# Optimization experiments

Measured on AMD Instinct MI355X. Metric: run time of the kernel, lower is better.

Reference implementation:

```python
import jax, jax.numpy as jnp
import numpy as np

N, F, E, LIN, C, B = 16384, 500, 128, 128, 10, 4096
P_EDGE = 0.002  # ~32 avg degree


def _l2norm(x):
    # F.normalize(dim=1), eps=1e-12
    n = jnp.linalg.norm(x, axis=1, keepdims=True)
    return x / jnp.maximum(n, 1e-12)


def setup_inputs() -> dict:
    key = jax.random.key(0)
    ks = jax.random.split(key, 10)
    adj = (jax.random.uniform(ks[0], (N, N)) < P_EDGE).astype(jnp.float32)
    idx = jnp.arange(N)
    adj = adj.at[idx, idx].set(1.0)  # self-loops guarantee degree >= 1
    data = jax.random.normal(ks[1], (N, F), dtype=jnp.float32)
    nodes = jax.random.randint(ks[2], (B,), 0, N)
    # Encoder 1: Linear(2F -> E); Encoder 2: Linear(2E -> E); classifier heads
    W1 = jax.random.normal(ks[3], (E, 2 * F), dtype=jnp.float32) * 0.03
    b1 = jnp.zeros((E,), jnp.float32)
    W2 = jax.random.normal(ks[4], (E, 2 * E), dtype=jnp.float32) * 0.06
    b2 = jnp.zeros((E,), jnp.float32)
    Wl1 = jax.random.normal(ks[5], (LIN, E), dtype=jnp.float32) * 0.08
    bl1 = jnp.zeros((LIN,), jnp.float32)
    Wl2 = jax.random.normal(ks[6], (C, LIN), dtype=jnp.float32) * 0.12
    bl2 = jnp.zeros((C,), jnp.float32)
    return {"nodes": nodes, "adj": adj, "data": data,
            "W1": W1, "b1": b1, "W2": W2, "b2": b2,
            "Wl1": Wl1, "bl1": bl1, "Wl2": Wl2, "bl2": bl2}


def reference(nodes, adj, data, W1, b1, W2, b2, Wl1, bl1, Wl2, bl2):
    deg = jnp.sum(adj, axis=1, keepdims=True)  # [N,1]
    # Layer 1 (mean aggregator over full neighbor set): computed for all nodes
    neigh1 = (adj @ data) / deg                               # [N,F]
    h1 = jnp.concatenate([data, neigh1], axis=1)              # [N,2F] (self, neigh)
    H1 = _l2norm(jax.nn.relu(h1 @ W1.T + b1))                 # [N,E]
    # Layer 2: only for the queried node batch
    neigh2 = (adj[nodes] @ H1) / deg[nodes]                   # [B,E]
    h2 = jnp.concatenate([H1[nodes], neigh2], axis=1)         # [B,2E]
    H2 = _l2norm(jax.nn.relu(h2 @ W2.T + b2))                 # [B,E]
    x = H2 @ Wl1.T + bl1                                      # [B,LIN]
    x = x @ Wl2.T + bl2                                       # [B,C]
    return jax.nn.softmax(x, axis=1)
```

## Files before the change

kernel.cpp:

```cpp
#include <hip/hip_runtime.h>
#include <math.h>
#include <stddef.h>

#define N_NODES 16384
#define F_DIM   500
#define KP1     512
#define E_DIM   128
#define C_DIM   10
#define B_DIM   4096
#define MAXDEG  128

typedef __attribute__((ext_vector_type(8))) short short8;
typedef __attribute__((ext_vector_type(4))) float f32x4;

__device__ inline unsigned short f2bf(float f) {
    union { float f; unsigned int u; } v; v.f = f;
    unsigned int u = v.u;
    u += 0x7FFFu + ((u >> 16) & 1u);
    return (unsigned short)(u >> 16);
}

__global__ __launch_bounds__(256) void k_prep(const float* __restrict__ W1,
                                              const float* __restrict__ W2,
                                              const float* __restrict__ Wl1,
                                              unsigned short* __restrict__ Wt1,
                                              unsigned short* __restrict__ Wt2,
                                              float* __restrict__ Wl1t) {
    const int bb = blockIdx.x;
    const int t = threadIdx.x;
    if (bb < 512) {
        int idx = bb * 256 + t;
        int n = idx >> 9, k = idx & 511;
        float v = (k < F_DIM) ? W1[(size_t)(n & 127) * 1000 + (n >> 7) * F_DIM + k] : 0.0f;
        Wt1[idx] = f2bf(v);
    } else if (bb < 640) {
        int idx = (bb - 512) * 256 + t;
        int n = idx >> 7, k = idx & 127;
        Wt2[idx] = f2bf(W2[(size_t)(n & 127) * 256 + (n >> 7) * 128 + k]);
    } else {
        __shared__ float tile[32][33];
        int tb = bb - 640;
        int k0 = (tb & 3) * 32, e0 = (tb >> 2) * 32;
        int tx = t & 31, ty0 = t >> 5;
#pragma unroll
        for (int q = 0; q < 4; ++q) {
            int ty = ty0 + q * 8;
            tile[ty][tx] = Wl1[(size_t)(e0 + ty) * 128 + k0 + tx];
        }
        __syncthreads();
#pragma unroll
        for (int q = 0; q < 4; ++q) {
            int ty = ty0 + q * 8;
            Wl1t[(size_t)(k0 + ty) * 128 + e0 + tx] = tile[tx][ty];
        }
    }
}

__global__ __launch_bounds__(256) void k_mix(const float* __restrict__ data,
                                             const unsigned short* __restrict__ Wt1,
                                             float* __restrict__ X,
                                             const float* __restrict__ adj,
                                             unsigned short* __restrict__ nbr,
                                             int* __restrict__ deg) {
    __shared__ alignas(16) unsigned char s_raw[(32 * 40 + 256 * 40) * 2];
    const int bb = blockIdx.x;
    const int tid = threadIdx.x;

    if (bb < 512) {
        unsigned short* sA = (unsigned short*)s_raw;
        unsigned short* sB = sA + 32 * 40;
        const int w    = tid >> 6;
        const int lane = tid & 63;
        const int l16  = lane & 15;
        const int quad = lane >> 4;
        const int blockM = bb * 32;
        f32x4 acc[2][4] = {};
#pragma unroll 1
        for (int c = 0; c < (KP1 >> 5); ++c) {
            const int k0 = c << 5;
            if (tid < 128) {
                int row = tid >> 2, cc = tid & 3;
                int kbase = k0 + cc * 8;
                const float* Arow = data + (size_t)(blockM + row) * F_DIM;
                float4 f0 = (kbase + 4 <= F_DIM) ? *(const float4*)(Arow + kbase)
                                                 : make_float4(0.f, 0.f, 0.f, 0.f);
                float4 f1 = (kbase + 8 <= F_DIM) ? *(const float4*)(Arow + kbase + 4)
                                                 : make_float4(0.f, 0.f, 0.f, 0.f);
                short8 v;
                v[0] = (short)f2bf(f0.x); v[1] = (short)f2bf(f0.y);
                v[2] = (short)f2bf(f0.z); v[3] = (short)f2bf(f0.w);
                v[4] = (short)f2bf(f1.x); v[5] = (short)f2bf(f1.y);
                v[6] = (short)f2bf(f1.z); v[7] = (short)f2bf(f1.w);
                *(short8*)(sA + row * 40 + cc * 8) = v;
            }
#pragma unroll
            for (int q = 0; q < 4; ++q) {
                int idx = tid + 256 * q;
                int row = idx >> 2, cc = idx & 3;
                short8 v = *(const short8*)(Wt1 + (size_t)row * KP1 + k0 + cc * 8);
                *(short8*)(sB + row * 40 + cc * 8) = v;
            }
            __syncthreads();
            short8 af[2], bf[4];
#pragma unroll
            for (int mt = 0; mt < 2; ++mt)
                af[mt] = *(const short8*)(sA + (mt * 16 + l16) * 40 + quad * 8);
#pragma unroll
            for (int nt = 0; nt < 4; ++nt)
                bf[nt] = *(const short8*)(sB + (w * 64 + nt * 16 + l16) * 40 + quad * 8);
#pragma unroll
            for (int mt = 0; mt < 2; ++mt)
#pragma unroll
                for (int nt = 0; nt < 4; ++nt)
                    acc[mt][nt] = __builtin_amdgcn_mfma_f32_16x16x32_bf16(af[mt], bf[nt], acc[mt][nt], 0, 0, 0);
            __syncthreads();
        }
#pragma unroll
        for (int mt = 0; mt < 2; ++mt)
#pragma unroll
            for (int nt = 0; nt < 4; ++nt) {
                int col = w * 64 + nt * 16 + l16;
#pragma unroll
                for (int r = 0; r < 4; ++r) {
                    int row = blockM + mt * 16 + quad * 4 + r;
                    X[(size_t)row * 256 + col] = acc[mt][nt][r];
                }
            }
    } else {
        const int i = bb - 512;
        int* s_cnt = (int*)s_raw;
        int* s_idx = ((int*)s_raw) + 4;
        const float4* row4 = (const float4*)(adj + (size_t)i * N_NODES);
        if (tid == 0) *s_cnt = 0;
        __syncthreads();
        float4 v[16];
#pragma unroll
        for (int p = 0; p < 16; ++p) v[p] = row4[p * 256 + tid];
#pragma unroll
        for (int p = 0; p < 16; ++p) {
            int col = p * 1024 + tid * 4;
            if (v[p].x != 0.f) { int q = atomicAdd(s_cnt, 1); if (q < MAXDEG) s_idx[q] = col;     }
            if (v[p].y != 0.f) { int q = atomicAdd(s_cnt, 1); if (q < MAXDEG) s_idx[q] = col + 1; }
            if (v[p].z != 0.f) { int q = atomicAdd(s_cnt, 1); if (q < MAXDEG) s_idx[q] = col + 2; }
            if (v[p].w != 0.f) { int q = atomicAdd(s_cnt, 1); if (q < MAXDEG) s_idx[q] = col + 3; }
        }
        __syncthreads();
        int cnt = *s_cnt; if (cnt > MAXDEG) cnt = MAXDEG;
        if (tid < cnt) nbr[(size_t)i * MAXDEG + tid] = (unsigned short)s_idx[tid];
        if (tid == 0) deg[i] = cnt;
    }
}

__global__ __launch_bounds__(256) void k_gather(const unsigned short* __restrict__ nbr,
                                                const int* __restrict__ deg,
                                                const float* __restrict__ X,
                                                const float* __restrict__ b1,
                                                unsigned short* __restrict__ H1b) {
    const int i = blockIdx.x;
    const int t = threadIdx.x;
    const int cnt = deg[i];
    __shared__ int s_idx[MAXDEG];
    __shared__ float s_part[8][128];
    __shared__ float s_w[2];
    if (t < cnt) s_idx[t] = nbr[(size_t)i * MAXDEG + t];
    __syncthreads();
    const int g = t >> 5, l = t & 31;
    float4 a4 = make_float4(0.f, 0.f, 0.f, 0.f);
    for (int k = g; k < cnt; k += 8) {
        float4 x4 = ((const float4*)(X + (size_t)s_idx[k] * 256 + 128))[l];
        a4.x += x4.x; a4.y += x4.y; a4.z += x4.z; a4.w += x4.w;
    }
    *(float4*)&s_part[g][l * 4] = a4;
    __syncthreads();
    float vv = 0.f;
    if (t < 128) {
        float tot = 0.f;
#pragma unroll
        for (int g2 = 0; g2 < 8; ++g2) tot += s_part[g2][t];
        vv = X[(size_t)i * 256 + t] + tot / (float)cnt + b1[t];
        vv = fmaxf(vv, 0.f);
        float s = vv * vv;
#pragma unroll
        for (int off = 32; off > 0; off >>= 1) s += __shfl_down(s, off, 64);
        if ((t & 63) == 0) s_w[t >> 6] = s;
    }
    __syncthreads();
    if (t < 128) {
        float denom = fmaxf(sqrtf(s_w[0] + s_w[1]), 1e-12f);
        H1b[(size_t)i * 128 + t] = f2bf(vv / denom);
    }
}

__global__ __launch_bounds__(256) void k_gemm_mfma(const unsigned short* __restrict__ A,
                                                   int K,
                                                   const unsigned short* __restrict__ B,
                                                   float* __restrict__ Cout) {
    __shared__ unsigned short sA[32 * 40];
    __shared__ unsigned short sB[256 * 40];
    const int tid  = threadIdx.x;
    const int w    = tid >> 6;
    const int lane = tid & 63;
    const int l16  = lane & 15;
    const int quad = lane >> 4;
    const int blockM = blockIdx.x * 32;
    f32x4 acc[2][4] = {};
    for (int c = 0; c < (K >> 5); ++c) {
        const int k0 = c << 5;
        if (tid < 128) {
            int row = tid >> 2, cc = tid & 3;
            short8 v = *(const short8*)(A + (size_t)(blockM + row) * K + k0 + cc * 8);
            *(short8*)(sA + row * 40 + cc * 8) = v;
        }
#pragma unroll
        for (int q = 0; q < 4; ++q) {
            int idx = tid + 256 * q;
            int row = idx >> 2, cc = idx & 3;
            short8 v = *(const short8*)(B + (size_t)row * K + k0 + cc * 8);
            *(short8*)(sB + row * 40 + cc * 8) = v;
        }
        __syncthreads();
        short8 af[2], bf[4];
#pragma unroll
        for (int mt = 0; mt < 2; ++mt)
            af[mt] = *(const short8*)(sA + (mt * 16 + l16) * 40 + quad * 8);
#pragma unroll
        for (int nt = 0; nt < 4; ++nt)
            bf[nt] = *(const short8*)(sB + (w * 64 + nt * 16 + l16) * 40 + quad * 8);
#pragma unroll
        for (int mt = 0; mt < 2; ++mt)
#pragma unroll
            for (int nt = 0; nt < 4; ++nt)
                acc[mt][nt] = __builtin_amdgcn_mfma_f32_16x16x32_bf16(af[mt], bf[nt], acc[mt][nt], 0, 0, 0);
        __syncthreads();
    }
#pragma unroll
    for (int mt = 0; mt < 2; ++mt)
#pragma unroll
        for (int nt = 0; nt < 4; ++nt) {
            int col = w * 64 + nt * 16 + l16;
#pragma unroll
            for (int r = 0; r < 4; ++r) {
                int row = blockM + mt * 16 + quad * 4 + r;
                Cout[(size_t)row * 256 + col] = acc[mt][nt][r];
            }
        }
}

__global__ __launch_bounds__(256) void k_l2head(const int* __restrict__ nodes,
                                                const unsigned short* __restrict__ nbr,
                                                const int* __restrict__ deg,
                                                const float* __restrict__ Y,
                                                const float* __restrict__ b2,
                                                const float* __restrict__ Wl1t,
                                                const float* __restrict__ bl1,
                                                const float* __restrict__ Wl2,
                                                const float* __restrict__ bl2,
                                                float* __restrict__ out) {
    const int b = blockIdx.x;
    const int t = threadIdx.x;
    const int n = nodes[b];
    const int cnt = deg[n];
    __shared__ int s_idx[MAXDEG];
    __shared__ float s_part[8][128];
    __shared__ float s_h[128];
    __shared__ float s_x[128];
    __shared__ float s_c[C_DIM];
    __shared__ float s_w[2];
    if (t < cnt) s_idx[t] = nbr[(size_t)n * MAXDEG + t];
    __syncthreads();
    const int g = t >> 5, l = t & 31;
    float4 a4 = make_float4(0.f, 0.f, 0.f, 0.f);
    for (int k = g; k < cnt; k += 8) {
        float4 y4 = ((const float4*)(Y + (size_t)s_idx[k] * 256 + 128))[l];
        a4.x += y4.x; a4.y += y4.y; a4.z += y4.z; a4.w += y4.w;
    }
    *(float4*)&s_part[g][l * 4] = a4;
    __syncthreads();
    if (t < 128) {
        float tot = 0.f;
#pragma unroll
        for (int g2 = 0; g2 < 8; ++g2) tot += s_part[g2][t];
        float vv = Y[(size_t)n * 256 + t] + tot / (float)cnt + b2[t];
        vv = fmaxf(vv, 0.f);
        float s = vv * vv;
#pragma unroll
        for (int off = 32; off > 0; off >>= 1) s += __shfl_down(s, off, 64);
        if ((t & 63) == 0) s_w[t >> 6] = s;
        __syncthreads();
        float denom = fmaxf(sqrtf(s_w[0] + s_w[1]), 1e-12f);
        s_h[t] = vv / denom;
    } else {
        __syncthreads();
    }
    __syncthreads();
    if (t < 128) {
        float x1 = bl1[t];
#pragma unroll 8
        for (int kk = 0; kk < 128; ++kk)
            x1 += Wl1t[kk * 128 + t] * s_h[kk];
        s_x[t] = x1;
    }
    __syncthreads();
    if (t < C_DIM) {
        float l2 = bl2[t];
        const float* wr = Wl2 + (size_t)t * 128;
        for (int kk = 0; kk < 128; ++kk) l2 += wr[kk] * s_x[kk];
        s_c[t] = l2;
    }
    __syncthreads();
    if (t < C_DIM) {
        float mx = -1e30f;
        for (int c = 0; c < C_DIM; ++c) mx = fmaxf(mx, s_c[c]);
        float se = 0.f;
        for (int c = 0; c < C_DIM; ++c) se += expf(s_c[c] - mx);
        out[(size_t)b * C_DIM + t] = expf(s_c[t] - mx) / se;
    }
}

extern "C" void kernel_launch(void* const* d_in, const int* in_sizes, int n_in,
                              void* d_out, int out_size, void* d_ws, size_t ws_size,
                              hipStream_t stream) {
    const int*   nodes = (const int*)  d_in[0];
    const float* adj   = (const float*)d_in[1];
    const float* data  = (const float*)d_in[2];
    const float* W1    = (const float*)d_in[3];
    const float* b1    = (const float*)d_in[4];
    const float* W2    = (const float*)d_in[5];
    const float* b2    = (const float*)d_in[6];
    const float* Wl1   = (const float*)d_in[7];
    const float* bl1   = (const float*)d_in[8];
    const float* Wl2   = (const float*)d_in[9];
    const float* bl2   = (const float*)d_in[10];
    float* out = (float*)d_out;

    unsigned short* Wt1 = (unsigned short*)d_ws;
    unsigned short* Wt2 = Wt1 + 256 * KP1;
    unsigned short* H1b = Wt2 + 256 * 128;
    float* Wl1t = (float*)(H1b + (size_t)N_NODES * 128);
    float* X    = Wl1t + 128 * 128;
    float* Y    = X    + (size_t)N_NODES * 256;
    unsigned short* nbr = (unsigned short*)(Y + (size_t)N_NODES * 256);
    int*   deg  = (int*)(nbr + (size_t)N_NODES * MAXDEG);

    k_prep<<<656, 256, 0, stream>>>(W1, W2, Wl1, Wt1, Wt2, Wl1t);

    k_mix   <<<512 + N_NODES, 256, 0, stream>>>(data, Wt1, X, adj, nbr, deg);
    k_gather<<<N_NODES, 256, 0, stream>>>(nbr, deg, X, b1, H1b);

    k_gemm_mfma<<<N_NODES / 32, 256, 0, stream>>>(H1b, E_DIM, Wt2, Y);
    k_l2head   <<<B_DIM, 256, 0, stream>>>(nodes, nbr, deg, Y, b2, Wl1t, bl1, Wl2, bl2, out);
}
```

Measured before the change: 1.423 ms.

## Compute layer-2 only for batch nodes by aggregating before the linear transform

Removes the full-graph layer-2 GEMM and instead aggregates bf16 H1 neighbours first, then applies the W2 self and neighbour halves as a per-node matvec inside the head kernel. The intermediate X is also stored in bf16 rather than fp32, halving its write and gather traffic. This trades a whole-graph GEMM and a large fp32 buffer for per-block fp32 matvec work over 4096 batch nodes, plus extra bf16 rounding of X.

```diff
diff --git a/kernel.cpp b/kernel.cpp
--- a/kernel.cpp
+++ b/kernel.cpp
@@ -19,12 +19,17 @@
     u += 0x7FFFu + ((u >> 16) & 1u);
     return (unsigned short)(u >> 16);
 }
+__device__ inline float bf2f(unsigned short u) {
+    union { unsigned int u; float f; } v; v.u = (unsigned int)u << 16;
+    return v.f;
+}
 
 __global__ __launch_bounds__(256) void k_prep(const float* __restrict__ W1,
                                               const float* __restrict__ W2,
                                               const float* __restrict__ Wl1,
                                               unsigned short* __restrict__ Wt1,
-                                              unsigned short* __restrict__ Wt2,
+                                              float* __restrict__ W2ta,
+                                              float* __restrict__ W2tb,
                                               float* __restrict__ Wl1t) {
     const int bb = blockIdx.x;
     const int t = threadIdx.x;
@@ -33,32 +38,32 @@
         int n = idx >> 9, k = idx & 511;
         float v = (k < F_DIM) ? W1[(size_t)(n & 127) * 1000 + (n >> 7) * F_DIM + k] : 0.0f;
         Wt1[idx] = f2bf(v);
-    } else if (bb < 640) {
-        int idx = (bb - 512) * 256 + t;
-        int n = idx >> 7, k = idx & 127;
-        Wt2[idx] = f2bf(W2[(size_t)(n & 127) * 256 + (n >> 7) * 128 + k]);
     } else {
+        const float* src; float* dst; int S, cOff;
+        int tb;
+        if (bb < 528)      { src = W2;  dst = W2ta; S = 256; cOff = 0;   tb = bb - 512; }
+        else if (bb < 544) { src = W2;  dst = W2tb; S = 256; cOff = 128; tb = bb - 528; }
+        else               { src = Wl1; dst = Wl1t; S = 128; cOff = 0;   tb = bb - 544; }
         __shared__ float tile[32][33];
-        int tb = bb - 640;
         int k0 = (tb & 3) * 32, e0 = (tb >> 2) * 32;
         int tx = t & 31, ty0 = t >> 5;
 #pragma unroll
         for (int q = 0; q < 4; ++q) {
             int ty = ty0 + q * 8;
-            tile[ty][tx] = Wl1[(size_t)(e0 + ty) * 128 + k0 + tx];
+            tile[ty][tx] = src[(size_t)(e0 + ty) * S + cOff + k0 + tx];
         }
         __syncthreads();
 #pragma unroll
         for (int q = 0; q < 4; ++q) {
             int ty = ty0 + q * 8;
-            Wl1t[(size_t)(k0 + ty) * 128 + e0 + tx] = tile[tx][ty];
+            dst[(size_t)(k0 + ty) * 128 + e0 + tx] = tile[tx][ty];
         }
     }
 }
 
 __global__ __launch_bounds__(256) void k_mix(const float* __restrict__ data,
                                              const unsigned short* __restrict__ Wt1,
-                                             float* __restrict__ X,
+                                             unsigned short* __restrict__ Xb16,
                                              const float* __restrict__ adj,
                                              unsigned short* __restrict__ nbr,
                                              int* __restrict__ deg) {
@@ -123,7 +128,7 @@
 #pragma unroll
                 for (int r = 0; r < 4; ++r) {
                     int row = blockM + mt * 16 + quad * 4 + r;
-                    X[(size_t)row * 256 + col] = acc[mt][nt][r];
+                    Xb16[(size_t)row * 256 + col] = f2bf(acc[mt][nt][r]);
                 }
             }
     } else {
@@ -153,7 +158,7 @@
 
 __global__ __launch_bounds__(256) void k_gather(const unsigned short* __restrict__ nbr,
                                                 const int* __restrict__ deg,
-                                                const float* __restrict__ X,
+                                                const unsigned short* __restrict__ Xb16,
                                                 const float* __restrict__ b1,
                                                 unsigned short* __restrict__ H1b) {
     const int i = blockIdx.x;
@@ -167,8 +172,8 @@
     const int g = t >> 5, l = t & 31;
     float4 a4 = make_float4(0.f, 0.f, 0.f, 0.f);
     for (int k = g; k < cnt; k += 8) {
-        float4 x4 = ((const float4*)(X + (size_t)s_idx[k] * 256 + 128))[l];
-        a4.x += x4.x; a4.y += x4.y; a4.z += x4.z; a4.w += x4.w;
+        ushort4 x4 = ((const ushort4*)(Xb16 + (size_t)s_idx[k] * 256 + 128))[l];
+        a4.x += bf2f(x4.x); a4.y += bf2f(x4.y); a4.z += bf2f(x4.z); a4.w += bf2f(x4.w);
     }
     *(float4*)&s_part[g][l * 4] = a4;
     __syncthreads();
@@ -177,7 +182,7 @@
         float tot = 0.f;
 #pragma unroll
         for (int g2 = 0; g2 < 8; ++g2) tot += s_part[g2][t];
-        vv = X[(size_t)i * 256 + t] + tot / (float)cnt + b1[t];
+        vv = bf2f(Xb16[(size_t)i * 256 + t]) + tot / (float)cnt + b1[t];
         vv = fmaxf(vv, 0.f);
         float s = vv * vv;
 #pragma unroll
@@ -189,67 +194,14 @@
         float denom = fmaxf(sqrtf(s_w[0] + s_w[1]), 1e-12f);
         H1b[(size_t)i * 128 + t] = f2bf(vv / denom);
     }
-}
-
-__global__ __launch_bounds__(256) void k_gemm_mfma(const unsigned short* __restrict__ A,
-                                                   int K,
-                                                   const unsigned short* __restrict__ B,
-                                                   float* __restrict__ Cout) {
-    __shared__ unsigned short sA[32 * 40];
-    __shared__ unsigned short sB[256 * 40];
-    const int tid  = threadIdx.x;
-    const int w    = tid >> 6;
-    const int lane = tid & 63;
-    const int l16  = lane & 15;
-    const int quad = lane >> 4;
-    const int blockM = blockIdx.x * 32;
-    f32x4 acc[2][4] = {};
-    for (int c = 0; c < (K >> 5); ++c) {
-        const int k0 = c << 5;
-        if (tid < 128) {
-            int row = tid >> 2, cc = tid & 3;
-            short8 v = *(const short8*)(A + (size_t)(blockM + row) * K + k0 + cc * 8);
-            *(short8*)(sA + row * 40 + cc * 8) = v;
-        }
-#pragma unroll
-        for (int q = 0; q < 4; ++q) {
-            int idx = tid + 256 * q;
-            int row = idx >> 2, cc = idx & 3;
-            short8 v = *(const short8*)(B + (size_t)row * K + k0 + cc * 8);
-            *(short8*)(sB + row * 40 + cc * 8) = v;
-        }
-        __syncthreads();
-        short8 af[2], bf[4];
-#pragma unroll
-        for (int mt = 0; mt < 2; ++mt)
-            af[mt] = *(const short8*)(sA + (mt * 16 + l16) * 40 + quad * 8);
-#pragma unroll
-        for (int nt = 0; nt < 4; ++nt)
-            bf[nt] = *(const short8*)(sB + (w * 64 + nt * 16 + l16) * 40 + quad * 8);
-#pragma unroll
-        for (int mt = 0; mt < 2; ++mt)
-#pragma unroll
-            for (int nt = 0; nt < 4; ++nt)
-                acc[mt][nt] = __builtin_amdgcn_mfma_f32_16x16x32_bf16(af[mt], bf[nt], acc[mt][nt], 0, 0, 0);
-        __syncthreads();
-    }
-#pragma unroll
-    for (int mt = 0; mt < 2; ++mt)
-#pragma unroll
-        for (int nt = 0; nt < 4; ++nt) {
-            int col = w * 64 + nt * 16 + l16;
-#pragma unroll
-            for (int r = 0; r < 4; ++r) {
-                int row = blockM + mt * 16 + quad * 4 + r;
-                Cout[(size_t)row * 256 + col] = acc[mt][nt][r];
-            }
-        }
 }
 
 __global__ __launch_bounds__(256) void k_l2head(const int* __restrict__ nodes,
                                                 const unsigned short* __restrict__ nbr,
                                                 const int* __restrict__ deg,
-                                                const float* __restrict__ Y,
+                                                const unsigned short* __restrict__ H1b,
+                                                const float* __restrict__ W2ta,
+                                                const float* __restrict__ W2tb,
                                                 const float* __restrict__ b2,
                                                 const float* __restrict__ Wl1t,
                                                 const float* __restrict__ bl1,
@@ -262,6 +214,8 @@
     const int cnt = deg[n];
     __shared__ int s_idx[MAXDEG];
     __shared__ float s_part[8][128];
+    __shared__ float s_hn[128];
+    __shared__ float s_m[128];
     __shared__ float s_h[128];
     __shared__ float s_x[128];
     __shared__ float s_c[C_DIM];
@@ -271,8 +225,8 @@
     const int g = t >> 5, l = t & 31;
     float4 a4 = make_float4(0.f, 0.f, 0.f, 0.f);
     for (int k = g; k < cnt; k += 8) {
-        float4 y4 = ((const float4*)(Y + (size_t)s_idx[k] * 256 + 128))[l];
-        a4.x += y4.x; a4.y += y4.y; a4.z += y4.z; a4.w += y4.w;
+        ushort4 h4 = ((const ushort4*)(H1b + (size_t)s_idx[k] * 128))[l];
+        a4.x += bf2f(h4.x); a4.y += bf2f(h4.y); a4.z += bf2f(h4.z); a4.w += bf2f(h4.w);
     }
     *(float4*)&s_part[g][l * 4] = a4;
     __syncthreads();
@@ -280,15 +234,23 @@
         float tot = 0.f;
 #pragma unroll
         for (int g2 = 0; g2 < 8; ++g2) tot += s_part[g2][t];
-        float vv = Y[(size_t)n * 256 + t] + tot / (float)cnt + b2[t];
-        vv = fmaxf(vv, 0.f);
-        float s = vv * vv;
+        s_m[t]  = tot / (float)cnt;
+        s_hn[t] = bf2f(H1b[(size_t)n * 128 + t]);
+    }
+    __syncthreads();
+    if (t < 128) {
+        float v = b2[t];
+#pragma unroll 4
+        for (int kk = 0; kk < 128; ++kk)
+            v += s_hn[kk] * W2ta[kk * 128 + t] + s_m[kk] * W2tb[kk * 128 + t];
+        v = fmaxf(v, 0.f);
+        float s = v * v;
 #pragma unroll
         for (int off = 32; off > 0; off >>= 1) s += __shfl_down(s, off, 64);
         if ((t & 63) == 0) s_w[t >> 6] = s;
         __syncthreads();
         float denom = fmaxf(sqrtf(s_w[0] + s_w[1]), 1e-12f);
-        s_h[t] = vv / denom;
+        s_h[t] = v / denom;
     } else {
         __syncthreads();
     }
@@ -333,20 +295,20 @@
     const float* bl2   = (const float*)d_in[10];
     float* out = (float*)d_out;
 
-    unsigned short* Wt1 = (unsigned short*)d_ws;
-    unsigned short* Wt2 = Wt1 + 256 * KP1;
-    unsigned short* H1b = Wt2 + 256 * 128;
-    float* Wl1t = (float*)(H1b + (size_t)N_NODES * 128);
-    float* X    = Wl1t + 128 * 128;
-    float* Y    = X    + (size_t)N_NODES * 256;
-    unsigned short* nbr = (unsigned short*)(Y + (size_t)N_NODES * 256);
-    int*   deg  = (int*)(nbr + (size_t)N_NODES * MAXDEG);
-
-    k_prep<<<656, 256, 0, stream>>>(W1, W2, Wl1, Wt1, Wt2, Wl1t);
-
-    k_mix   <<<512 + N_NODES, 256, 0, stream>>>(data, Wt1, X, adj, nbr, deg);
-    k_gather<<<N_NODES, 256, 0, stream>>>(nbr, deg, X, b1, H1b);
-
-    k_gemm_mfma<<<N_NODES / 32, 256, 0, stream>>>(H1b, E_DIM, Wt2, Y);
-    k_l2head   <<<B_DIM, 256, 0, stream>>>(nodes, nbr, deg, Y, b2, Wl1t, bl1, Wl2, bl2, out);
-}
+    float* W2ta = (float*)d_ws;
+    float* W2tb = W2ta + 16384;
+    float* Wl1t = W2tb + 16384;
+    unsigned short* Wt1  = (unsigned short*)(Wl1t + 16384);
+    unsigned short* Xb16 = Wt1 + 256 * KP1;
+    unsigned short* H1b  = Xb16 + (size_t)N_NODES * 256;
+    unsigned short* nbr  = H1b + (size_t)N_NODES * 128;
+    int* deg = (int*)(nbr + (size_t)N_NODES * MAXDEG);
+
+    k_prep<<<560, 256, 0, stream>>>(W1, W2, Wl1, Wt1, W2ta, W2tb, Wl1t);
+
+    k_mix   <<<512 + N_NODES, 256, 0, stream>>>(data, Wt1, Xb16, adj, nbr, deg);
+    k_gather<<<N_NODES, 256, 0, stream>>>(nbr, deg, Xb16, b1, H1b);
+
+    k_l2head<<<B_DIM, 256, 0, stream>>>(nodes, nbr, deg, H1b, W2ta, W2tb, b2,
+                                        Wl1t, bl1, Wl2, bl2, out);
+}
```

New measurement: 1.450 ms. Within noise of the previous version (+1.9%).

## Store intermediates in bf16 and compute layer-2 self projection only for batch nodes

Applied to the files above, without the earlier changes.

The first-layer projection X and the second-layer neighbour projection are now stored as bf16 instead of fp32, which halves the bytes read in the two gather kernels. The second-layer GEMM is split so that the neighbour half runs over all nodes while the self half runs only over the 4096 queried nodes (gathered by index), and its output is written to a compact fp32 buffer. This removes redundant self-projection work and memory traffic. The cost is bf16 rounding error in the aggregated features.

```diff
diff --git a/kernel.cpp b/kernel.cpp
--- a/kernel.cpp
+++ b/kernel.cpp
@@ -19,12 +19,17 @@
     u += 0x7FFFu + ((u >> 16) & 1u);
     return (unsigned short)(u >> 16);
 }
+__device__ inline float bf2f(unsigned short u) {
+    union { unsigned int u; float f; } v; v.u = (unsigned int)u << 16;
+    return v.f;
+}
 
 __global__ __launch_bounds__(256) void k_prep(const float* __restrict__ W1,
                                               const float* __restrict__ W2,
                                               const float* __restrict__ Wl1,
                                               unsigned short* __restrict__ Wt1,
-                                              unsigned short* __restrict__ Wt2,
+                                              unsigned short* __restrict__ W2ab16,
+                                              unsigned short* __restrict__ W2bb16,
                                               float* __restrict__ Wl1t) {
     const int bb = blockIdx.x;
     const int t = threadIdx.x;
@@ -33,10 +38,14 @@
         int n = idx >> 9, k = idx & 511;
         float v = (k < F_DIM) ? W1[(size_t)(n & 127) * 1000 + (n >> 7) * F_DIM + k] : 0.0f;
         Wt1[idx] = f2bf(v);
-    } else if (bb < 640) {
+    } else if (bb < 576) {
         int idx = (bb - 512) * 256 + t;
         int n = idx >> 7, k = idx & 127;
-        Wt2[idx] = f2bf(W2[(size_t)(n & 127) * 256 + (n >> 7) * 128 + k]);
+        W2ab16[idx] = f2bf(W2[(size_t)n * 256 + k]);
+    } else if (bb < 640) {
+        int idx = (bb - 576) * 256 + t;
+        int n = idx >> 7, k = idx & 127;
+        W2bb16[idx] = f2bf(W2[(size_t)n * 256 + 128 + k]);
     } else {
         __shared__ float tile[32][33];
         int tb = bb - 640;
@@ -58,7 +67,7 @@
 
 __global__ __launch_bounds__(256) void k_mix(const float* __restrict__ data,
                                              const unsigned short* __restrict__ Wt1,
-                                             float* __restrict__ X,
+                                             unsigned short* __restrict__ Xb16,
                                              const float* __restrict__ adj,
                                              unsigned short* __restrict__ nbr,
                                              int* __restrict__ deg) {
@@ -123,7 +132,7 @@
 #pragma unroll
                 for (int r = 0; r < 4; ++r) {
                     int row = blockM + mt * 16 + quad * 4 + r;
-                    X[(size_t)row * 256 + col] = acc[mt][nt][r];
+                    Xb16[(size_t)row * 256 + col] = f2bf(acc[mt][nt][r]);
                 }
             }
     } else {
@@ -153,7 +162,7 @@
 
 __global__ __launch_bounds__(256) void k_gather(const unsigned short* __restrict__ nbr,
                                                 const int* __restrict__ deg,
-                                                const float* __restrict__ X,
+                                                const unsigned short* __restrict__ Xb16,
                                                 const float* __restrict__ b1,
                                                 unsigned short* __restrict__ H1b) {
     const int i = blockIdx.x;
@@ -167,8 +176,8 @@
     const int g = t >> 5, l = t & 31;
     float4 a4 = make_float4(0.f, 0.f, 0.f, 0.f);
     for (int k = g; k < cnt; k += 8) {
-        float4 x4 = ((const float4*)(X + (size_t)s_idx[k] * 256 + 128))[l];
-        a4.x += x4.x; a4.y += x4.y; a4.z += x4.z; a4.w += x4.w;
+        ushort4 x4 = ((const ushort4*)(Xb16 + (size_t)s_idx[k] * 256 + 128))[l];
+        a4.x += bf2f(x4.x); a4.y += bf2f(x4.y); a4.z += bf2f(x4.z); a4.w += bf2f(x4.w);
     }
     *(float4*)&s_part[g][l * 4] = a4;
     __syncthreads();
@@ -177,7 +186,7 @@
         float tot = 0.f;
 #pragma unroll
         for (int g2 = 0; g2 < 8; ++g2) tot += s_part[g2][t];
-        vv = X[(size_t)i * 256 + t] + tot / (float)cnt + b1[t];
+        vv = bf2f(Xb16[(size_t)i * 256 + t]) + tot / (float)cnt + b1[t];
         vv = fmaxf(vv, 0.f);
         float s = vv * vv;
 #pragma unroll
@@ -191,57 +200,66 @@
     }
 }
 
-__global__ __launch_bounds__(256) void k_gemm_mfma(const unsigned short* __restrict__ A,
-                                                   int K,
-                                                   const unsigned short* __restrict__ B,
-                                                   float* __restrict__ Cout) {
+__global__ __launch_bounds__(256) void k_gemm2(const unsigned short* __restrict__ H1b,
+                                               const unsigned short* __restrict__ W2bb16,
+                                               const unsigned short* __restrict__ W2ab16,
+                                               const int* __restrict__ nodes,
+                                               unsigned short* __restrict__ Yb16,
+                                               float* __restrict__ Ya) {
     __shared__ unsigned short sA[32 * 40];
-    __shared__ unsigned short sB[256 * 40];
+    __shared__ unsigned short sB[128 * 40];
+    const int bb = blockIdx.x;
+    const bool selfp = (bb >= 512);
+    const unsigned short* B = selfp ? W2ab16 : W2bb16;
+    const int blockM = (selfp ? (bb - 512) : bb) * 32;
     const int tid  = threadIdx.x;
     const int w    = tid >> 6;
     const int lane = tid & 63;
     const int l16  = lane & 15;
     const int quad = lane >> 4;
-    const int blockM = blockIdx.x * 32;
-    f32x4 acc[2][4] = {};
-    for (int c = 0; c < (K >> 5); ++c) {
+    f32x4 acc[2][2] = {};
+#pragma unroll
+    for (int c = 0; c < 4; ++c) {
         const int k0 = c << 5;
         if (tid < 128) {
             int row = tid >> 2, cc = tid & 3;
-            short8 v = *(const short8*)(A + (size_t)(blockM + row) * K + k0 + cc * 8);
+            int m = blockM + row;
+            int src = selfp ? nodes[m] : m;
+            short8 v = *(const short8*)(H1b + (size_t)src * 128 + k0 + cc * 8);
             *(short8*)(sA + row * 40 + cc * 8) = v;
         }
 #pragma unroll
-        for (int q = 0; q < 4; ++q) {
+        for (int q = 0; q < 2; ++q) {
             int idx = tid + 256 * q;
             int row = idx >> 2, cc = idx & 3;
-            short8 v = *(const short8*)(B + (size_t)row * K + k0 + cc * 8);
+            short8 v = *(const short8*)(B + (size_t)row * 128 + k0 + cc * 8);
             *(short8*)(sB + row * 40 + cc * 8) = v;
         }
         __syncthreads();
-        short8 af[2], bf[4];
+        short8 af[2], bf[2];
 #pragma unroll
         for (int mt = 0; mt < 2; ++mt)
             af[mt] = *(const short8*)(sA + (mt * 16 + l16) * 40 + quad * 8);
 #pragma unroll
-        for (int nt = 0; nt < 4; ++nt)
-            bf[nt] = *(const short8*)(sB + (w * 64 + nt * 16 + l16) * 40 + quad * 8);
+        for (int nt = 0; nt < 2; ++nt)
+            bf[nt] = *(const short8*)(sB + (w * 32 + nt * 16 + l16) * 40 + quad * 8);
 #pragma unroll
         for (int mt = 0; mt < 2; ++mt)
 #pragma unroll
-            for (int nt = 0; nt < 4; ++nt)
+            for (int nt = 0; nt < 2; ++nt)
                 acc[mt][nt] = __builtin_amdgcn_mfma_f32_16x16x32_bf16(af[mt], bf[nt], acc[mt][nt], 0, 0, 0);
         __syncthreads();
     }
 #pragma unroll
     for (int mt = 0; mt < 2; ++mt)
 #pragma unroll
-        for (int nt = 0; nt < 4; ++nt) {
-            int col = w * 64 + nt * 16 + l16;
+        for (int nt = 0; nt < 2; ++nt) {
+            int col = w * 32 + nt * 16 + l16;
 #pragma unroll
             for (int r = 0; r < 4; ++r) {
                 int row = blockM + mt * 16 + quad * 4 + r;
-                Cout[(size_t)row * 256 + col] = acc[mt][nt][r];
+                if (selfp) Ya[(size_t)row * 128 + col] = acc[mt][nt][r];
+                else       Yb16[(size_t)row * 128 + col] = f2bf(acc[mt][nt][r]);
             }
         }
 }
@@ -249,7 +267,8 @@
 __global__ __launch_bounds__(256) void k_l2head(const int* __restrict__ nodes,
                                                 const unsigned short* __restrict__ nbr,
                                                 const int* __restrict__ deg,
-                                                const float* __restrict__ Y,
+                                                const unsigned short* __restrict__ Yb16,
+                                                const float* __restrict__ Ya,
                                                 const float* __restrict__ b2,
                                                 const float* __restrict__ Wl1t,
                                                 const float* __restrict__ bl1,
@@ -271,26 +290,27 @@
     const int g = t >> 5, l = t & 31;
     float4 a4 = make_float4(0.f, 0.f, 0.f, 0.f);
     for (int k = g; k < cnt; k += 8) {
-        float4 y4 = ((const float4*)(Y + (size_t)s_idx[k] * 256 + 128))[l];
-        a4.x += y4.x; a4.y += y4.y; a4.z += y4.z; a4.w += y4.w;
+        ushort4 y4 = ((const ushort4*)(Yb16 + (size_t)s_idx[k] * 128))[l];
+        a4.x += bf2f(y4.x); a4.y += bf2f(y4.y); a4.z += bf2f(y4.z); a4.w += bf2f(y4.w);
     }
     *(float4*)&s_part[g][l * 4] = a4;
     __syncthreads();
+    float vv = 0.f;
     if (t < 128) {
         float tot = 0.f;
 #pragma unroll
         for (int g2 = 0; g2 < 8; ++g2) tot += s_part[g2][t];
-        float vv = Y[(size_t)n * 256 + t] + tot / (float)cnt + b2[t];
+        vv = Ya[(size_t)b * 128 + t] + tot / (float)cnt + b2[t];
         vv = fmaxf(vv, 0.f);
         float s = vv * vv;
 #pragma unroll
         for (int off = 32; off > 0; off >>= 1) s += __shfl_down(s, off, 64);
         if ((t & 63) == 0) s_w[t >> 6] = s;
-        __syncthreads();
+    }
+    __syncthreads();
+    if (t < 128) {
         float denom = fmaxf(sqrtf(s_w[0] + s_w[1]), 1e-12f);
         s_h[t] = vv / denom;
-    } else {
-        __syncthreads();
     }
     __syncthreads();
     if (t < 128) {
@@ -333,20 +353,24 @@
     const float* bl2   = (const float*)d_in[10];
     float* out = (float*)d_out;
 
-    unsigned short* Wt1 = (unsigned short*)d_ws;
-    unsigned short* Wt2 = Wt1 + 256 * KP1;
-    unsigned short* H1b = Wt2 + 256 * 128;
-    float* Wl1t = (float*)(H1b + (size_t)N_NODES * 128);
-    float* X    = Wl1t + 128 * 128;
-    float* Y    = X    + (size_t)N_NODES * 256;
-    unsigned short* nbr = (unsigned short*)(Y + (size_t)N_NODES * 256);
-    int*   deg  = (int*)(nbr + (size_t)N_NODES * MAXDEG);
-
-    k_prep<<<656, 256, 0, stream>>>(W1, W2, Wl1, Wt1, Wt2, Wl1t);
-
-    k_mix   <<<512 + N_NODES, 256, 0, stream>>>(data, Wt1, X, adj, nbr, deg);
-    k_gather<<<N_NODES, 256, 0, stream>>>(nbr, deg, X, b1, H1b);
-
-    k_gemm_mfma<<<N_NODES / 32, 256, 0, stream>>>(H1b, E_DIM, Wt2, Y);
-    k_l2head   <<<B_DIM, 256, 0, stream>>>(nodes, nbr, deg, Y, b2, Wl1t, bl1, Wl2, bl2, out);
-}
+    float* Wl1t = (float*)d_ws;
+    float* Ya   = Wl1t + 16384;
+    unsigned short* Wt1    = (unsigned short*)(Ya + (size_t)B_DIM * 128);
+    unsigned short* W2ab16 = Wt1 + 256 * KP1;
+    unsigned short* W2bb16 = W2ab16 + 16384;
+    unsigned short* Xb16   = W2bb16 + 16384;
+    unsigned short* H1b    = Xb16 + (size_t)N_NODES * 256;
+    unsigned short* Yb16   = H1b + (size_t)N_NODES * 128;
+    unsigned short* nbr    = Yb16 + (size_t)N_NODES * 128;
+    int* deg = (int*)(nbr + (size_t)N_NODES * MAXDEG);
+
+    k_prep<<<656, 256, 0, stream>>>(W1, W2, Wl1, Wt1, W2ab16, W2bb16, Wl1t);
+
+    k_mix   <<<512 + N_NODES, 256, 0, stream>>>(data, Wt1, Xb16, adj, nbr, deg);
+    k_gather<<<N_NODES, 256, 0, stream>>>(nbr, deg, Xb16, b1, H1b);
+
+    k_gemm2 <<<512 + 128, 256, 0, stream>>>(H1b, W2bb16, W2ab16, nodes, Yb16, Ya);
+
+    k_l2head<<<B_DIM, 256, 0, stream>>>(nodes, nbr, deg, Yb16, Ya, b2,
+                                        Wl1t, bl1, Wl2, bl2, out);
+}
```

Result: no change. 1.417 ms (-0.4%).
